# Kernel optimization log

Hardware: AMD Instinct MI355X
Metric: run time of the kernel (lower is better)

## Reference

```python
import jax, jax.numpy as jnp
import numpy as np

TWO_PI = 2.0 * np.pi
SMOOTH = 0.12  # smoothing_factor default

N_STATIONS = 100000
N_TIME = 1000
K = 8


def _spatial_smooth(param, idx, w, is_phase=False, s=SMOOTH):
    # param: [N] (or [N,C]); idx: [N,K] int; w: [N,K] row-normalized
    nb = param[idx]  # [N,K] or [N,K,C]
    if param.ndim == 2:
        w = w[..., None]
    if is_phase:
        # circular mean via unit-complex average, expressed with real atan2
        re = (1.0 - s) * jnp.cos(param) + s * jnp.sum(w * jnp.cos(nb), axis=1)
        im = (1.0 - s) * jnp.sin(param) + s * jnp.sum(w * jnp.sin(nb), axis=1)
        return jnp.arctan2(im, re)
    return (1.0 - s) * param + s * jnp.sum(w * nb, axis=1)


def setup_inputs() -> dict:
    key = jax.random.key(0)
    ks = jax.random.split(key, 10)
    time_vector = jnp.arange(N_TIME, dtype=jnp.float32) / 365.25  # years
    constant_offset = jnp.zeros((N_STATIONS,), jnp.float32)
    linear_trend = jax.random.normal(ks[0], (N_STATIONS,), jnp.float32) * 5.0
    seasonal_amplitudes = jnp.ones((N_STATIONS, 3), jnp.float32) * 8.0
    seasonal_phases = jax.random.uniform(ks[1], (N_STATIONS, 3), jnp.float32) * TWO_PI
    residual_amplitudes = jnp.ones((N_STATIONS, 2), jnp.float32) * 1.5
    residual_phases = jax.random.uniform(ks[2], (N_STATIONS, 2), jnp.float32) * TWO_PI
    residual_periods = jnp.array([180.0, 730.0], jnp.float32)
    periods = jnp.array([0.25, 0.5, 1.0], jnp.float32)
    neighbor_indices = jax.random.randint(ks[3], (N_STATIONS, K), 0, N_STATIONS)
    raw_w = jax.random.uniform(ks[4], (N_STATIONS, K), jnp.float32)
    neighbor_weights = raw_w / (jnp.sum(raw_w, axis=1, keepdims=True) + 1e-6)
    return {
        "time_vector": time_vector,
        "constant_offset": constant_offset,
        "linear_trend": linear_trend,
        "seasonal_amplitudes": seasonal_amplitudes,
        "seasonal_phases": seasonal_phases,
        "residual_amplitudes": residual_amplitudes,
        "residual_phases": residual_phases,
        "residual_periods": residual_periods,
        "periods": periods,
        "neighbor_indices": neighbor_indices,
        "neighbor_weights": neighbor_weights,
    }


def reference(time_vector, constant_offset, linear_trend, seasonal_amplitudes,
              seasonal_phases, residual_amplitudes, residual_phases,
              residual_periods, periods, neighbor_indices, neighbor_weights):
    t = time_vector[None, :]  # [1,T] broadcast over stations
    signals = constant_offset[:, None] + linear_trend[:, None] * t  # [N,T]
    # batched spatial smoothing across all 3 seasonal channels at once
    sm_amp = _spatial_smooth(seasonal_amplitudes, neighbor_indices, neighbor_weights)            # [N,3]
    sm_phase = _spatial_smooth(seasonal_phases, neighbor_indices, neighbor_weights, is_phase=True)  # [N,3]
    for i in range(3):  # fixed small set of periods
        freq = 1.0 / periods[i]
        signals = signals + sm_amp[:, i:i+1] * jnp.sin(TWO_PI * freq * t + sm_phase[:, i:i+1])
    for i in range(2):
        freq = 1.0 / residual_periods[i]
        signals = signals + residual_amplitudes[:, i:i+1] * jnp.sin(TWO_PI * freq * t + residual_phases[:, i:i+1])
    return signals
```

## Files before the change

### kernel.cpp

```cpp
#include <hip/hip_runtime.h>

typedef float f32x4 __attribute__((ext_vector_type(4)));

#define NSEAS 3
#define NRES  2
#define NCOMP 5
#define KNB   8
#define TWO_PI_F 6.28318530717958647692f
#define SPB 48
#define BSIG 256


__global__ void build_tables_kernel(
    const float* __restrict__ time_vector,
    const float* __restrict__ periods,
    const float* __restrict__ res_periods,
    float* __restrict__ sinT,
    float* __restrict__ cosT,
    int T)
{
    int t = blockIdx.x * blockDim.x + threadIdx.x;
    if (t >= T) return;
    float tt = time_vector[t];
    #pragma unroll
    for (int c = 0; c < NCOMP; ++c) {
        float f = (c < NSEAS) ? (1.0f / periods[c])
                              : (1.0f / res_periods[c - NSEAS]);
        float s, co;
        __sincosf(TWO_PI_F * f * tt, &s, &co);
        sinT[c * T + t] = s;
        cosT[c * T + t] = co;
    }
}

__global__ void smooth_params_kernel(
    const float* __restrict__ constant_offset,
    const float* __restrict__ linear_trend,
    const float* __restrict__ seas_amp,
    const float* __restrict__ seas_phase,
    const float* __restrict__ res_amp,
    const float* __restrict__ res_phase,
    const int*   __restrict__ nb_idx,
    const float* __restrict__ nb_w,
    float* __restrict__ params,
    int N)
{
    int st = blockIdx.x * blockDim.x + threadIdx.x;
    if (st >= N) return;

    const float S = 0.12f, OMS = 1.0f - 0.12f;

    const int4*  ip = reinterpret_cast<const int4*>(nb_idx + st * KNB);
    const f32x4* wp = reinterpret_cast<const f32x4*>(nb_w + st * KNB);
    int4  i0 = ip[0], i1 = ip[1];
    f32x4 w0 = wp[0], w1 = wp[1];
    int   idx[KNB] = {i0.x, i0.y, i0.z, i0.w, i1.x, i1.y, i1.z, i1.w};
    float w[KNB]   = {w0.x, w0.y, w0.z, w0.w, w1.x, w1.y, w1.z, w1.w};

    float accA[NSEAS]  = {0.f, 0.f, 0.f};
    float accRe[NSEAS] = {0.f, 0.f, 0.f};
    float accIm[NSEAS] = {0.f, 0.f, 0.f};

    #pragma unroll
    for (int k = 0; k < KNB; ++k) {
        int nb = idx[k];
        #pragma unroll
        for (int i = 0; i < NSEAS; ++i) {
            float a = seas_amp[nb * NSEAS + i];
            float p = seas_phase[nb * NSEAS + i];
            float sp, cp;
            __sincosf(p, &sp, &cp);
            accA[i]  = fmaf(w[k], a,  accA[i]);
            accRe[i] = fmaf(w[k], cp, accRe[i]);
            accIm[i] = fmaf(w[k], sp, accIm[i]);
        }
    }

    float outp[12];
    outp[0] = constant_offset[st];
    outp[1] = linear_trend[st];

    #pragma unroll
    for (int i = 0; i < NSEAS; ++i) {
        float smA = OMS * seas_amp[st * NSEAS + i] + S * accA[i];
        float sp, cp;
        __sincosf(seas_phase[st * NSEAS + i], &sp, &cp);
        float re = OMS * cp + S * accRe[i];
        float im = OMS * sp + S * accIm[i];
        float r   = sqrtf(re * re + im * im);
        float inv = smA / fmaxf(r, 1e-30f);
        outp[2 + 2 * i] = re * inv;
        outp[3 + 2 * i] = im * inv;
    }

    #pragma unroll
    for (int i = 0; i < NRES; ++i) {
        float a = res_amp[st * NRES + i];
        float sp, cp;
        __sincosf(res_phase[st * NRES + i], &sp, &cp);
        outp[2 + 2 * (NSEAS + i)] = a * cp;
        outp[3 + 2 * (NSEAS + i)] = a * sp;
    }

    f32x4* po = reinterpret_cast<f32x4*>(params + (size_t)st * 12);
    po[0] = f32x4{outp[0], outp[1], outp[2],  outp[3]};
    po[1] = f32x4{outp[4], outp[5], outp[6],  outp[7]};
    po[2] = f32x4{outp[8], outp[9], outp[10], outp[11]};
}

__global__ __launch_bounds__(BSIG) void signals_kernel(
    const float* __restrict__ time_vector,
    const float* __restrict__ params,
    const float* __restrict__ sinT,
    const float* __restrict__ cosT,
    float* __restrict__ out,
    int N, int T, int spb)
{
    int tid = threadIdx.x;
    int t0  = tid * 4;
    bool active = (t0 + 3) < T;

    float tv[4];
    float sT[NCOMP][4], cT[NCOMP][4];
    if (active) {
        f32x4 t4 = *reinterpret_cast<const f32x4*>(time_vector + t0);
        tv[0] = t4.x; tv[1] = t4.y; tv[2] = t4.z; tv[3] = t4.w;
        #pragma unroll
        for (int c = 0; c < NCOMP; ++c) {
            f32x4 s4 = *reinterpret_cast<const f32x4*>(sinT + c * T + t0);
            f32x4 c4 = *reinterpret_cast<const f32x4*>(cosT + c * T + t0);
            sT[c][0] = s4.x; sT[c][1] = s4.y; sT[c][2] = s4.z; sT[c][3] = s4.w;
            cT[c][0] = c4.x; cT[c][1] = c4.y; cT[c][2] = c4.z; cT[c][3] = c4.w;
        }
    }

    int stBeg = blockIdx.x * spb;
    int stEnd = min(stBeg + spb, N);
    int st = stBeg;

    for (; st + 4 <= stEnd; st += 4) {
        float off[4], trend[4], cs[4][NCOMP], cc[4][NCOMP];
        #pragma unroll
        for (int u = 0; u < 4; ++u) {
            const f32x4* p = reinterpret_cast<const f32x4*>(params + (size_t)(st + u) * 12);
            f32x4 P0 = p[0], P1 = p[1], P2 = p[2];
            off[u] = P0.x; trend[u] = P0.y;
            cs[u][0] = P0.z; cc[u][0] = P0.w;
            cs[u][1] = P1.x; cc[u][1] = P1.y;
            cs[u][2] = P1.z; cc[u][2] = P1.w;
            cs[u][3] = P2.x; cc[u][3] = P2.y;
            cs[u][4] = P2.z; cc[u][4] = P2.w;
        }
        if (active) {
            #pragma unroll
            for (int u = 0; u < 4; ++u) {
                float v[4];
                #pragma unroll
                for (int j = 0; j < 4; ++j) {
                    float acc = fmaf(trend[u], tv[j], off[u]);
                    #pragma unroll
                    for (int i = 0; i < NCOMP; ++i) {
                        acc = fmaf(cs[u][i], sT[i][j], acc);
                        acc = fmaf(cc[u][i], cT[i][j], acc);
                    }
                    v[j] = acc;
                }
                f32x4 o = {v[0], v[1], v[2], v[3]};
                *reinterpret_cast<f32x4*>(out + (size_t)(st + u) * T + t0) = o;
            }
        }
    }

    for (; st < stEnd; ++st) {
        const f32x4* p = reinterpret_cast<const f32x4*>(params + (size_t)st * 12);
        f32x4 P0 = p[0], P1 = p[1], P2 = p[2];
        float off = P0.x, trend = P0.y;
        float cs[NCOMP], cc[NCOMP];
        cs[0] = P0.z; cc[0] = P0.w;
        cs[1] = P1.x; cc[1] = P1.y;
        cs[2] = P1.z; cc[2] = P1.w;
        cs[3] = P2.x; cc[3] = P2.y;
        cs[4] = P2.z; cc[4] = P2.w;
        if (active) {
            float v[4];
            #pragma unroll
            for (int j = 0; j < 4; ++j) {
                float acc = fmaf(trend, tv[j], off);
                #pragma unroll
                for (int i = 0; i < NCOMP; ++i) {
                    acc = fmaf(cs[i], sT[i][j], acc);
                    acc = fmaf(cc[i], cT[i][j], acc);
                }
                v[j] = acc;
            }
            f32x4 o = {v[0], v[1], v[2], v[3]};
            *reinterpret_cast<f32x4*>(out + (size_t)st * T + t0) = o;
        } else if (t0 < T) {
            for (int j = 0; j < 4 && t0 + j < T; ++j) {
                int t = t0 + j;
                float acc = fmaf(trend, time_vector[t], off);
                for (int i = 0; i < NCOMP; ++i) {
                    acc = fmaf(cs[i], sinT[i * T + t], acc);
                    acc = fmaf(cc[i], cosT[i * T + t], acc);
                }
                out[(size_t)st * T + t] = acc;
            }
        }
    }
}

extern "C" void kernel_launch(void* const* d_in, const int* in_sizes, int n_in,
                              void* d_out, int out_size, void* d_ws, size_t ws_size,
                              hipStream_t stream) {
    const float* time_vector     = (const float*)d_in[0];
    const float* constant_offset = (const float*)d_in[1];
    const float* linear_trend    = (const float*)d_in[2];
    const float* seas_amp        = (const float*)d_in[3];
    const float* seas_phase      = (const float*)d_in[4];
    const float* res_amp         = (const float*)d_in[5];
    const float* res_phase       = (const float*)d_in[6];
    const float* res_periods     = (const float*)d_in[7];
    const float* periods         = (const float*)d_in[8];
    const int*   nb_idx          = (const int*)d_in[9];
    const float* nb_w            = (const float*)d_in[10];

    int T = in_sizes[0];
    int N = in_sizes[1];

    float* params = (float*)d_ws;
    float* sinT   = params + (size_t)N * 12;
    float* cosT   = sinT + (size_t)NCOMP * T;
    float* out    = (float*)d_out;

    {
        int threads = 256;
        int blocks  = (T + threads - 1) / threads;
        build_tables_kernel<<<blocks, threads, 0, stream>>>(
            time_vector, periods, res_periods, sinT, cosT, T);
    }

    {
        int threads = 256;
        int blocks  = (N + threads - 1) / threads;
        smooth_params_kernel<<<blocks, threads, 0, stream>>>(
            constant_offset, linear_trend, seas_amp, seas_phase,
            res_amp, res_phase, nb_idx, nb_w, params, N);
    }

    {
        int spb  = SPB;
        int grid = (N + spb - 1) / spb;
        signals_kernel<<<grid, BSIG, 0, stream>>>(
            time_vector, params, sinT, cosT, out, N, T, spb);
    }
}
```

Baseline: 111.5 us.

## Fuse table build, neighbor smoothing and signal synthesis into one kernel

Merges the three kernels into one. Each block computes the smoothed parameters for its stations into shared memory, with one thread per station (every fifth thread), and each thread computes the sin/cos time tables in registers instead of reading them from a precomputed global table. This removes two kernel launches and the global round trip for the parameter and table buffers. In exchange, every block repeats the table sincos work, the smoothing step runs on only a few threads per block before a barrier, and stations per block changes from 48 to 50.

```diff
diff --git a/kernel.cpp b/kernel.cpp
--- a/kernel.cpp
+++ b/kernel.cpp
@@ -7,118 +7,97 @@
 #define NCOMP 5
 #define KNB   8
 #define TWO_PI_F 6.28318530717958647692f
-#define SPB 48
+#define SPB  50
 #define BSIG 256
 
-
-__global__ void build_tables_kernel(
+__global__ __launch_bounds__(BSIG) void fused_insar_kernel(
     const float* __restrict__ time_vector,
-    const float* __restrict__ periods,
-    const float* __restrict__ res_periods,
-    float* __restrict__ sinT,
-    float* __restrict__ cosT,
-    int T)
-{
-    int t = blockIdx.x * blockDim.x + threadIdx.x;
-    if (t >= T) return;
-    float tt = time_vector[t];
-    #pragma unroll
-    for (int c = 0; c < NCOMP; ++c) {
-        float f = (c < NSEAS) ? (1.0f / periods[c])
-                              : (1.0f / res_periods[c - NSEAS]);
-        float s, co;
-        __sincosf(TWO_PI_F * f * tt, &s, &co);
-        sinT[c * T + t] = s;
-        cosT[c * T + t] = co;
-    }
-}
-
-__global__ void smooth_params_kernel(
     const float* __restrict__ constant_offset,
     const float* __restrict__ linear_trend,
     const float* __restrict__ seas_amp,
     const float* __restrict__ seas_phase,
     const float* __restrict__ res_amp,
     const float* __restrict__ res_phase,
+    const float* __restrict__ res_periods,
+    const float* __restrict__ periods,
     const int*   __restrict__ nb_idx,
     const float* __restrict__ nb_w,
-    float* __restrict__ params,
-    int N)
+    float* __restrict__ out,
+    int N, int T)
 {
-    int st = blockIdx.x * blockDim.x + threadIdx.x;
-    if (st >= N) return;
-
-    const float S = 0.12f, OMS = 1.0f - 0.12f;
-
-    const int4*  ip = reinterpret_cast<const int4*>(nb_idx + st * KNB);
-    const f32x4* wp = reinterpret_cast<const f32x4*>(nb_w + st * KNB);
-    int4  i0 = ip[0], i1 = ip[1];
-    f32x4 w0 = wp[0], w1 = wp[1];
-    int   idx[KNB] = {i0.x, i0.y, i0.z, i0.w, i1.x, i1.y, i1.z, i1.w};
-    float w[KNB]   = {w0.x, w0.y, w0.z, w0.w, w1.x, w1.y, w1.z, w1.w};
-
-    float accA[NSEAS]  = {0.f, 0.f, 0.f};
-    float accRe[NSEAS] = {0.f, 0.f, 0.f};
-    float accIm[NSEAS] = {0.f, 0.f, 0.f};
-
-    #pragma unroll
-    for (int k = 0; k < KNB; ++k) {
-        int nb = idx[k];
-        #pragma unroll
-        for (int i = 0; i < NSEAS; ++i) {
-            float a = seas_amp[nb * NSEAS + i];
-            float p = seas_phase[nb * NSEAS + i];
-            float sp, cp;
-            __sincosf(p, &sp, &cp);
-            accA[i]  = fmaf(w[k], a,  accA[i]);
-            accRe[i] = fmaf(w[k], cp, accRe[i]);
-            accIm[i] = fmaf(w[k], sp, accIm[i]);
-        }
-    }
-
-    float outp[12];
-    outp[0] = constant_offset[st];
-    outp[1] = linear_trend[st];
-
-    #pragma unroll
-    for (int i = 0; i < NSEAS; ++i) {
-        float smA = OMS * seas_amp[st * NSEAS + i] + S * accA[i];
-        float sp, cp;
-        __sincosf(seas_phase[st * NSEAS + i], &sp, &cp);
-        float re = OMS * cp + S * accRe[i];
-        float im = OMS * sp + S * accIm[i];
-        float r   = sqrtf(re * re + im * im);
-        float inv = smA / fmaxf(r, 1e-30f);
-        outp[2 + 2 * i] = re * inv;
-        outp[3 + 2 * i] = im * inv;
-    }
-
-    #pragma unroll
-    for (int i = 0; i < NRES; ++i) {
-        float a = res_amp[st * NRES + i];
-        float sp, cp;
-        __sincosf(res_phase[st * NRES + i], &sp, &cp);
-        outp[2 + 2 * (NSEAS + i)] = a * cp;
-        outp[3 + 2 * (NSEAS + i)] = a * sp;
-    }
-
-    f32x4* po = reinterpret_cast<f32x4*>(params + (size_t)st * 12);
-    po[0] = f32x4{outp[0], outp[1], outp[2],  outp[3]};
-    po[1] = f32x4{outp[4], outp[5], outp[6],  outp[7]};
-    po[2] = f32x4{outp[8], outp[9], outp[10], outp[11]};
-}
-
-__global__ __launch_bounds__(BSIG) void signals_kernel(
-    const float* __restrict__ time_vector,
-    const float* __restrict__ params,
-    const float* __restrict__ sinT,
-    const float* __restrict__ cosT,
-    float* __restrict__ out,
-    int N, int T, int spb)
-{
-    int tid = threadIdx.x;
-    int t0  = tid * 4;
-    bool active = (t0 + 3) < T;
+    __shared__ __align__(16) float sp[SPB * 12];
+
+    const int tid   = threadIdx.x;
+    const int stBeg = blockIdx.x * SPB;
+    const int nst   = min(SPB, N - stBeg);
+
+    {
+        int s = tid / 5;
+        if (tid == s * 5 && s < nst) {
+            int st = stBeg + s;
+            const float S = 0.12f, OMS = 1.0f - 0.12f;
+
+            const int4*  ip = reinterpret_cast<const int4*>(nb_idx + st * KNB);
+            const f32x4* wp = reinterpret_cast<const f32x4*>(nb_w + st * KNB);
+            int4  i0 = ip[0], i1 = ip[1];
+            f32x4 w0 = wp[0], w1 = wp[1];
+            int   idx[KNB] = {i0.x, i0.y, i0.z, i0.w, i1.x, i1.y, i1.z, i1.w};
+            float w[KNB]   = {w0.x, w0.y, w0.z, w0.w, w1.x, w1.y, w1.z, w1.w};
+
+            float accA[NSEAS]  = {0.f, 0.f, 0.f};
+            float accRe[NSEAS] = {0.f, 0.f, 0.f};
+            float accIm[NSEAS] = {0.f, 0.f, 0.f};
+
+            #pragma unroll
+            for (int k = 0; k < KNB; ++k) {
+                int nb = idx[k];
+                #pragma unroll
+                for (int i = 0; i < NSEAS; ++i) {
+                    float a = seas_amp[nb * NSEAS + i];
+                    float p = seas_phase[nb * NSEAS + i];
+                    float spn, cpn;
+                    __sincosf(p, &spn, &cpn);
+                    accA[i]  = fmaf(w[k], a,   accA[i]);
+                    accRe[i] = fmaf(w[k], cpn, accRe[i]);
+                    accIm[i] = fmaf(w[k], spn, accIm[i]);
+                }
+            }
+
+            float outp[12];
+            outp[0] = constant_offset[st];
+            outp[1] = linear_trend[st];
+
+            #pragma unroll
+            for (int i = 0; i < NSEAS; ++i) {
+                float smA = OMS * seas_amp[st * NSEAS + i] + S * accA[i];
+                float spn, cpn;
+                __sincosf(seas_phase[st * NSEAS + i], &spn, &cpn);
+                float re = OMS * cpn + S * accRe[i];
+                float im = OMS * spn + S * accIm[i];
+                float r   = sqrtf(re * re + im * im);
+                float inv = smA / fmaxf(r, 1e-30f);
+                outp[2 + 2 * i] = re * inv;
+                outp[3 + 2 * i] = im * inv;
+            }
+
+            #pragma unroll
+            for (int i = 0; i < NRES; ++i) {
+                float a = res_amp[st * NRES + i];
+                float spn, cpn;
+                __sincosf(res_phase[st * NRES + i], &spn, &cpn);
+                outp[2 + 2 * (NSEAS + i)] = a * cpn;
+                outp[3 + 2 * (NSEAS + i)] = a * spn;
+            }
+
+            f32x4* po = reinterpret_cast<f32x4*>(sp + s * 12);
+            po[0] = f32x4{outp[0], outp[1], outp[2],  outp[3]};
+            po[1] = f32x4{outp[4], outp[5], outp[6],  outp[7]};
+            po[2] = f32x4{outp[8], outp[9], outp[10], outp[11]};
+        }
+    }
+
+    const int t0 = tid * 4;
+    const bool active = (t0 + 3) < T;
 
     float tv[4];
     float sT[NCOMP][4], cT[NCOMP][4];
@@ -127,23 +106,26 @@
         tv[0] = t4.x; tv[1] = t4.y; tv[2] = t4.z; tv[3] = t4.w;
         #pragma unroll
         for (int c = 0; c < NCOMP; ++c) {
-            f32x4 s4 = *reinterpret_cast<const f32x4*>(sinT + c * T + t0);
-            f32x4 c4 = *reinterpret_cast<const f32x4*>(cosT + c * T + t0);
-            sT[c][0] = s4.x; sT[c][1] = s4.y; sT[c][2] = s4.z; sT[c][3] = s4.w;
-            cT[c][0] = c4.x; cT[c][1] = c4.y; cT[c][2] = c4.z; cT[c][3] = c4.w;
-        }
-    }
-
-    int stBeg = blockIdx.x * spb;
-    int stEnd = min(stBeg + spb, N);
-    int st = stBeg;
-
-    for (; st + 4 <= stEnd; st += 4) {
+            float f = (c < NSEAS) ? (1.0f / periods[c])
+                                  : (1.0f / res_periods[c - NSEAS]);
+            float wc = TWO_PI_F * f;
+            #pragma unroll
+            for (int j = 0; j < 4; ++j) {
+                __sincosf(wc * tv[j], &sT[c][j], &cT[c][j]);
+            }
+        }
+    }
+
+    __syncthreads();
+
+    int s = 0;
+
+    for (; s + 4 <= nst; s += 4) {
         float off[4], trend[4], cs[4][NCOMP], cc[4][NCOMP];
         #pragma unroll
         for (int u = 0; u < 4; ++u) {
-            const f32x4* p = reinterpret_cast<const f32x4*>(params + (size_t)(st + u) * 12);
-            f32x4 P0 = p[0], P1 = p[1], P2 = p[2];
+            const f32x4* pv = reinterpret_cast<const f32x4*>(sp + (s + u) * 12);
+            f32x4 P0 = pv[0], P1 = pv[1], P2 = pv[2];
             off[u] = P0.x; trend[u] = P0.y;
             cs[u][0] = P0.z; cc[u][0] = P0.w;
             cs[u][1] = P1.x; cc[u][1] = P1.y;
@@ -166,14 +148,14 @@
                     v[j] = acc;
                 }
                 f32x4 o = {v[0], v[1], v[2], v[3]};
-                *reinterpret_cast<f32x4*>(out + (size_t)(st + u) * T + t0) = o;
-            }
-        }
-    }
-
-    for (; st < stEnd; ++st) {
-        const f32x4* p = reinterpret_cast<const f32x4*>(params + (size_t)st * 12);
-        f32x4 P0 = p[0], P1 = p[1], P2 = p[2];
+                *reinterpret_cast<f32x4*>(out + (size_t)(stBeg + s + u) * T + t0) = o;
+            }
+        }
+    }
+
+    for (; s < nst; ++s) {
+        const f32x4* pv = reinterpret_cast<const f32x4*>(sp + s * 12);
+        f32x4 P0 = pv[0], P1 = pv[1], P2 = pv[2];
         float off = P0.x, trend = P0.y;
         float cs[NCOMP], cc[NCOMP];
         cs[0] = P0.z; cc[0] = P0.w;
@@ -181,6 +163,7 @@
         cs[2] = P1.z; cc[2] = P1.w;
         cs[3] = P2.x; cc[3] = P2.y;
         cs[4] = P2.z; cc[4] = P2.w;
+
         if (active) {
             float v[4];
             #pragma unroll
@@ -194,16 +177,21 @@
                 v[j] = acc;
             }
             f32x4 o = {v[0], v[1], v[2], v[3]};
-            *reinterpret_cast<f32x4*>(out + (size_t)st * T + t0) = o;
+            *reinterpret_cast<f32x4*>(out + (size_t)(stBeg + s) * T + t0) = o;
         } else if (t0 < T) {
             for (int j = 0; j < 4 && t0 + j < T; ++j) {
                 int t = t0 + j;
-                float acc = fmaf(trend, time_vector[t], off);
+                float tt = time_vector[t];
+                float acc = fmaf(trend, tt, off);
                 for (int i = 0; i < NCOMP; ++i) {
-                    acc = fmaf(cs[i], sinT[i * T + t], acc);
-                    acc = fmaf(cc[i], cosT[i * T + t], acc);
-                }
-                out[(size_t)st * T + t] = acc;
+                    float f = (i < NSEAS) ? (1.0f / periods[i])
+                                          : (1.0f / res_periods[i - NSEAS]);
+                    float sv, cv;
+                    __sincosf(TWO_PI_F * f * tt, &sv, &cv);
+                    acc = fmaf(cs[i], sv, acc);
+                    acc = fmaf(cc[i], cv, acc);
+                }
+                out[(size_t)(stBeg + s) * T + t] = acc;
             }
         }
     }
@@ -216,7 +204,7 @@
     const float* constant_offset = (const float*)d_in[1];
     const float* linear_trend    = (const float*)d_in[2];
     const float* seas_amp        = (const float*)d_in[3];
-    const float* seas_phase      = (const float*)d_in[4];
+    const float* seas_phase     = (const float*)d_in[4];
     const float* res_amp         = (const float*)d_in[5];
     const float* res_phase       = (const float*)d_in[6];
     const float* res_periods     = (const float*)d_in[7];
@@ -227,30 +215,12 @@
     int T = in_sizes[0];
     int N = in_sizes[1];
 
-    float* params = (float*)d_ws;
-    float* sinT   = params + (size_t)N * 12;
-    float* cosT   = sinT + (size_t)NCOMP * T;
-    float* out    = (float*)d_out;
-
-    {
-        int threads = 256;
-        int blocks  = (T + threads - 1) / threads;
-        build_tables_kernel<<<blocks, threads, 0, stream>>>(
-            time_vector, periods, res_periods, sinT, cosT, T);
-    }
-
-    {
-        int threads = 256;
-        int blocks  = (N + threads - 1) / threads;
-        smooth_params_kernel<<<blocks, threads, 0, stream>>>(
-            constant_offset, linear_trend, seas_amp, seas_phase,
-            res_amp, res_phase, nb_idx, nb_w, params, N);
-    }
-
-    {
-        int spb  = SPB;
-        int grid = (N + spb - 1) / spb;
-        signals_kernel<<<grid, BSIG, 0, stream>>>(
-            time_vector, params, sinT, cosT, out, N, T, spb);
-    }
+    float* out = (float*)d_out;
+
+    int grid = (N + SPB - 1) / SPB;
+    fused_insar_kernel<<<grid, BSIG, 0, stream>>>(
+        time_vector, constant_offset, linear_trend,
+        seas_amp, seas_phase, res_amp, res_phase,
+        res_periods, periods, nb_idx, nb_w,
+        out, N, T);
 }
```

New measurement: 97.28 us. 12.8% less time.
